# Kernel tuning notes

Hardware: AMD Instinct MI355X
Metric: run time of the kernel (lower is better)

## Reference

```python
import jax, jax.numpy as jnp
import numpy as np

DIM = 128


def setup_inputs() -> dict:
    key = jax.random.key(0)
    k1, k2, k3, k4 = jax.random.split(key, 4)
    x = jax.random.normal(k1, (8, 32768, DIM), dtype=jnp.float32)
    # nn.Linear(dim, dim*3, bias=False): weight applied as x @ W.T; store as [dim, 3*dim]
    W_qkv = jax.random.normal(k2, (DIM, 3 * DIM), dtype=jnp.float32) * (DIM ** -0.5)
    W_out = jax.random.normal(k3, (DIM, DIM), dtype=jnp.float32) * (DIM ** -0.5)
    b_out = jax.random.normal(k4, (DIM,), dtype=jnp.float32) * 0.01
    return {"x": x, "W_qkv": W_qkv, "W_out": W_out, "b_out": b_out}


def reference(x, W_qkv, W_out, b_out):
    dim = x.shape[-1]
    scale = dim ** -0.5
    qkv = x @ W_qkv  # [b, n, 3d]
    q, k, v = jnp.split(qkv, 3, axis=-1)
    q = jax.nn.softmax(q, axis=-1) * scale
    k = jax.nn.softmax(k, axis=-1)
    v = jax.nn.softmax(v, axis=-1)
    context = jnp.einsum('bnd,bne->bde', q, k)  # [b, d, d]
    out = jnp.einsum('bde,bne->bnd', context, v)  # [b, n, d]
    return out @ W_out + b_out
```

## Files before the change

### kernel.cpp

```cpp
#include <hip/hip_runtime.h>

#define SEQ 32768
#define QSCALE 0.08838834764831845f

typedef __attribute__((ext_vector_type(8))) short short8;
typedef __attribute__((ext_vector_type(8))) __bf16 bf16x8;
typedef __attribute__((ext_vector_type(16))) float f32x16;
typedef __attribute__((ext_vector_type(4))) float f32x4;
typedef __attribute__((ext_vector_type(4))) int int4v;
typedef __attribute__((ext_vector_type(2))) int int2v;

#define SWZ(r, c) ((((r) << 7) + (c)) ^ (((r) & 7) << 3))

__device__ __forceinline__ int cvtpk(float lo, float hi) {
  int r;
  asm("v_cvt_pk_bf16_f32 %0, %1, %2" : "=v"(r) : "v"(lo), "v"(hi));
  return r;
}

__device__ __forceinline__ f32x16 mfma_ii(int4v a, int4v b, f32x16 c) {
  return __builtin_amdgcn_mfma_f32_32x32x16_bf16(
      __builtin_bit_cast(bf16x8, a), __builtin_bit_cast(bf16x8, b), c, 0, 0, 0);
}

__device__ __forceinline__ int4v build_frag(float e0, float e1, float e2, float e3,
                                            float e4, float e5, float e6, float e7,
                                            int hi) {
  int t0 = cvtpk(e0, e1), t1 = cvtpk(e2, e3);
  int t2 = cvtpk(e4, e5), t3 = cvtpk(e6, e7);
  const int u0 = __shfl_xor(t2, 32), u1 = __shfl_xor(t3, 32);
  const int u2 = __shfl_xor(t0, 32), u3 = __shfl_xor(t1, 32);
  int4v f;
  f[0] = hi ? u0 : t0;
  f[1] = hi ? u1 : t1;
  f[2] = hi ? t2 : u2;
  f[3] = hi ? t3 : u3;
  return f;
}

__global__ void la_prep(const float* __restrict__ Wqkv, int4v* __restrict__ Wf) {
  const int fid = blockIdx.x * 256 + threadIdx.x;
  if (fid >= 6144) return;
  const int side = fid >> 11;
  const int rem = fid & 2047;
  const int tile = rem >> 9;
  const int ks = (rem >> 6) & 7;
  const int lane = rem & 63;
  const int k0 = ks * 16 + ((lane >> 5) << 3);
  const int col = side * 128 + tile * 32 + (lane & 31);
  int4v f;
  #pragma unroll
  for (int a = 0; a < 4; ++a)
    f[a] = cvtpk(Wqkv[(k0 + 2 * a) * 384 + col], Wqkv[(k0 + 2 * a + 1) * 384 + col]);
  Wf[fid] = f;
}

__global__ __launch_bounds__(1024, 4)
void la_pass1(const float* __restrict__ x, const int4v* __restrict__ Wf,
              float* __restrict__ partials, int strips, int nch) {
  __shared__ __align__(16) short xs[2][64 * 128];
  __shared__ int4v fragbuf[2][2][4][4][64];
  __shared__ __align__(16) float sumbuf[2][2][2][32][4];

  const int tid = threadIdx.x;
  const int lane = tid & 63;
  const int wv = tid >> 6;
  const int l31 = lane & 31;
  const int hi = lane >> 5;
  const int koff = hi << 3;
  const int h = wv >> 3;
  const int c = (wv >> 1) & 3;
  const int rh = wv & 1;
  const int td = wv >> 2;
  const int te = wv & 3;
  const float qs = h ? 1.0f : QSCALE;
  const int b = blockIdx.x / strips;
  const int strip = blockIdx.x - b * strips;
  const long base = (long)b * SEQ + (long)strip * (nch * 64);

  int4v wf[8];
  #pragma unroll
  for (int ks = 0; ks < 8; ++ks)
    wf[ks] = Wf[((((h << 2) + c) << 3) + ks) * 64 + lane];

  const int lr = tid >> 4;
  const int cf = (tid & 15) << 3;
  {
    const float* xp = x + (base + lr) * 128 + cf;
    f32x4 u0 = *(const f32x4*)xp;
    f32x4 u1 = *(const f32x4*)(xp + 4);
    int4v p;
    p[0] = cvtpk(u0[0], u0[1]); p[1] = cvtpk(u0[2], u0[3]);
    p[2] = cvtpk(u1[0], u1[1]); p[3] = cvtpk(u1[2], u1[3]);
    *(int4v*)&xs[0][SWZ(lr, cf)] = p;
  }
  __syncthreads();

  f32x16 ctx = {0.f};
  const int r0 = rh << 5;
  for (int i = 0; i < nch; ++i) {
    const int cur = i & 1;
    const int inx = (i + 1 < nch) ? i + 1 : i;
    const float* xp = x + (base + inx * 64 + lr) * 128 + cf;
    f32x4 u0 = *(const f32x4*)xp;
    f32x4 u1 = *(const f32x4*)(xp + 4);

    f32x16 acc = {0.f};
    #pragma unroll
    for (int ks = 0; ks < 8; ++ks) {
      const int4v xf = *(const int4v*)&xs[cur][SWZ(r0 + l31, (ks << 4) + koff)];
      acc = mfma_ii(wf[ks], xf, acc);
    }
    {
      float sa = 0.f, sb = 0.f;
      #pragma unroll
      for (int r = 0; r < 16; r += 2) { sa += __expf(acc[r]); sb += __expf(acc[r + 1]); }
      float s = sa + sb;
      s += __shfl_xor(s, 32);
      if (!hi) sumbuf[cur][h][rh][l31][c] = s;
    }

    acc = f32x16{0.f};
    #pragma unroll
    for (int ks = 0; ks < 8; ++ks) {
      const int4v xf = *(const int4v*)&xs[cur][SWZ(r0 + l31, (ks << 4) + koff)];
      acc = mfma_ii(xf, wf[ks], acc);
    }
    #pragma unroll
    for (int r = 0; r < 16; ++r) acc[r] = __expf(acc[r]);

    {
      int4v p;
      p[0] = cvtpk(u0[0], u0[1]); p[1] = cvtpk(u0[2], u0[3]);
      p[2] = cvtpk(u1[0], u1[1]); p[3] = cvtpk(u1[2], u1[3]);
      *(int4v*)&xs[cur ^ 1][SWZ(lr, cf)] = p;
    }
    __syncthreads();

    #pragma unroll
    for (int r = 0; r < 16; ++r) {
      const int n = (r & 3) + ((r >> 2) << 3) + (hi << 2);
      const f32x4 sv = *(const f32x4*)&sumbuf[cur][h][rh][n][0];
      acc[r] *= qs * __builtin_amdgcn_rcpf(sv[0] + sv[1] + sv[2] + sv[3]);
    }
    fragbuf[cur][h][c][(rh << 1) + 0][lane] =
        build_frag(acc[0], acc[1], acc[2], acc[3], acc[4], acc[5], acc[6], acc[7], hi);
    fragbuf[cur][h][c][(rh << 1) + 1][lane] =
        build_frag(acc[8], acc[9], acc[10], acc[11], acc[12], acc[13], acc[14], acc[15], hi);

    if (i > 0) {
      const int pb = cur ^ 1;
      #pragma unroll
      for (int ks = 0; ks < 4; ++ks)
        ctx = mfma_ii(fragbuf[pb][0][td][ks][lane], fragbuf[pb][1][te][ks][lane], ctx);
    }
  }
  __syncthreads();
  {
    const int pb = (nch - 1) & 1;
    #pragma unroll
    for (int ks = 0; ks < 4; ++ks)
      ctx = mfma_ii(fragbuf[pb][0][td][ks][lane], fragbuf[pb][1][te][ks][lane], ctx);
  }

  float* pout = partials + (long)blockIdx.x * 16384;
  #pragma unroll
  for (int r = 0; r < 16; ++r) {
    const int drow = (td << 5) + (r & 3) + ((r >> 2) << 3) + (hi << 2);
    pout[(drow << 7) + (te << 5) + l31] = ctx[r];
  }
}

__global__ void la_reduce(const float* __restrict__ partials, float* __restrict__ ctx,
                          int strips) {
  const int b = blockIdx.x >> 4;
  const int sl = blockIdx.x & 15;
  const int idx = (sl << 10) + ((int)threadIdx.x << 2);
  f32x4 acc = {0.f};
  for (int st = 0; st < strips; ++st)
    acc += *(const f32x4*)(partials + ((long)(b * strips + st) << 14) + idx);
  *(f32x4*)(ctx + ((long)b << 14) + idx) = acc;
}

__global__ void la_mkern(const float* __restrict__ ctx, const float* __restrict__ Wout,
                         int4v* __restrict__ Mtf) {
  __shared__ __align__(16) float cl[128 * 132];
  __shared__ float wo[128 * 32];
  const int tid = threadIdx.x;
  const int b = blockIdx.x >> 2;
  const int d0 = (blockIdx.x & 3) << 5;
  const float* cp = ctx + ((long)b << 14);
  for (int i = tid << 2; i < 16384; i += 1024) {
    f32x4 v = *(const f32x4*)(cp + i);
    *(f32x4*)&cl[(i >> 7) * 132 + (i & 127)] = v;
  }
  for (int i = tid; i < 128 * 32; i += 256)
    wo[i] = Wout[((i >> 5) << 7) + d0 + (i & 31)];
  __syncthreads();
  const int dq = tid >> 3;
  const int e0 = (tid & 7) << 4;
  float acc[16];
  #pragma unroll
  for (int i = 0; i < 16; ++i) acc[i] = 0.0f;
  for (int d = 0; d < 128; ++d) {
    const float w = wo[(d << 5) + dq];
    const float* cr = &cl[d * 132 + e0];
    #pragma unroll
    for (int i = 0; i < 16; ++i) acc[i] += cr[i] * w;
  }
  const int dp = d0 + dq;
  const int j = dp & 3, l = dp >> 2, ks = e0 >> 4;
  int4v lo, hi2;
  lo[0] = cvtpk(acc[0], acc[1]);   lo[1] = cvtpk(acc[2], acc[3]);
  lo[2] = cvtpk(acc[4], acc[5]);   lo[3] = cvtpk(acc[6], acc[7]);
  hi2[0] = cvtpk(acc[8], acc[9]);  hi2[1] = cvtpk(acc[10], acc[11]);
  hi2[2] = cvtpk(acc[12], acc[13]); hi2[3] = cvtpk(acc[14], acc[15]);
  int4v* dst = Mtf + ((((long)b << 2) + j) * 8 + ks) * 64;
  dst[l] = lo;
  dst[32 + l] = hi2;
}

__global__ __launch_bounds__(256, 3)
void la_pass2(const float* __restrict__ x, const int4v* __restrict__ Wf,
              const int4v* __restrict__ Mtf, const float* __restrict__ bout,
              float* __restrict__ out) {
  __shared__ __align__(16) short xs[4][32 * 128];

  const int tid = threadIdx.x;
  const int lane = tid & 63;
  const int wv = tid >> 6;
  const int l31 = lane & 31;
  const int hi = lane >> 5;
  const int koff = hi << 3;
  const int b = blockIdx.x >> 8;
  const int chunk = blockIdx.x & 255;
  const long row0 = (long)b * SEQ + (long)chunk * 128 + (wv << 5);

  {
    const float* xb = x + row0 * 128;
    f32x4 u[16];
    #pragma unroll
    for (int t = 0; t < 16; ++t)
      u[t] = *(const f32x4*)(xb + t * 256 + lane * 4);
    #pragma unroll
    for (int t = 0; t < 16; ++t) {
      const int flat = t * 256 + lane * 4;
      int2v w;
      w[0] = cvtpk(u[t][0], u[t][1]);
      w[1] = cvtpk(u[t][2], u[t][3]);
      *(int2v*)&xs[wv][SWZ(flat >> 7, flat & 127)] = w;
    }
  }
  const f32x4 bias = *(const f32x4*)(bout + (l31 << 2));
  asm volatile("s_waitcnt lgkmcnt(0)" ::: "memory");
  __builtin_amdgcn_sched_barrier(0);

  int4v xfr[8];
  #pragma unroll
  for (int ks = 0; ks < 8; ++ks)
    xfr[ks] = *(const int4v*)&xs[wv][SWZ(l31, (ks << 4) + koff)];

  const int4v* WvT = Wf + 2 * 2048;
  f32x16 a0 = {0.f}, a1 = {0.f}, a2 = {0.f}, a3 = {0.f};
  #pragma unroll
  for (int ks = 0; ks < 8; ++ks) {
    a0 = mfma_ii(WvT[(0 * 8 + ks) * 64 + lane], xfr[ks], a0);
    a1 = mfma_ii(WvT[(1 * 8 + ks) * 64 + lane], xfr[ks], a1);
    a2 = mfma_ii(WvT[(2 * 8 + ks) * 64 + lane], xfr[ks], a2);
    a3 = mfma_ii(WvT[(3 * 8 + ks) * 64 + lane], xfr[ks], a3);
  }

  float s = 0.f;
  #pragma unroll
  for (int r = 0; r < 16; ++r) {
    a0[r] = __expf(a0[r]); s += a0[r];
    a1[r] = __expf(a1[r]); s += a1[r];
    a2[r] = __expf(a2[r]); s += a2[r];
    a3[r] = __expf(a3[r]); s += a3[r];
  }
  s += __shfl_xor(s, 32);
  const float inv = __builtin_amdgcn_rcpf(s);
  #pragma unroll
  for (int r = 0; r < 16; ++r) {
    a0[r] *= inv; a1[r] *= inv; a2[r] *= inv; a3[r] *= inv;
  }

  int4v vf[8];
  vf[0] = build_frag(a0[0], a0[1], a0[2], a0[3], a0[4], a0[5], a0[6], a0[7], hi);
  vf[1] = build_frag(a0[8], a0[9], a0[10], a0[11], a0[12], a0[13], a0[14], a0[15], hi);
  vf[2] = build_frag(a1[0], a1[1], a1[2], a1[3], a1[4], a1[5], a1[6], a1[7], hi);
  vf[3] = build_frag(a1[8], a1[9], a1[10], a1[11], a1[12], a1[13], a1[14], a1[15], hi);
  vf[4] = build_frag(a2[0], a2[1], a2[2], a2[3], a2[4], a2[5], a2[6], a2[7], hi);
  vf[5] = build_frag(a2[8], a2[9], a2[10], a2[11], a2[12], a2[13], a2[14], a2[15], hi);
  vf[6] = build_frag(a3[0], a3[1], a3[2], a3[3], a3[4], a3[5], a3[6], a3[7], hi);
  vf[7] = build_frag(a3[8], a3[9], a3[10], a3[11], a3[12], a3[13], a3[14], a3[15], hi);

  const int4v* MtB = Mtf + ((long)b << 11);
  f32x16 o0 = {0.f}, o1 = {0.f}, o2 = {0.f}, o3 = {0.f};
  #pragma unroll
  for (int ks = 0; ks < 8; ++ks) {
    o0 = mfma_ii(vf[ks], MtB[(0 * 8 + ks) * 64 + lane], o0);
    o1 = mfma_ii(vf[ks], MtB[(1 * 8 + ks) * 64 + lane], o1);
    o2 = mfma_ii(vf[ks], MtB[(2 * 8 + ks) * 64 + lane], o2);
    o3 = mfma_ii(vf[ks], MtB[(3 * 8 + ks) * 64 + lane], o3);
  }

  float* obase = out + row0 * 128 + (l31 << 2);
  #pragma unroll
  for (int r = 0; r < 16; ++r) {
    const int n = (r & 3) + ((r >> 2) << 3) + (hi << 2);
    f32x4 v;
    v[0] = o0[r] + bias[0];
    v[1] = o1[r] + bias[1];
    v[2] = o2[r] + bias[2];
    v[3] = o3[r] + bias[3];
    *(f32x4*)(obase + (long)n * 128) = v;
  }
}

extern "C" void kernel_launch(void* const* d_in, const int* in_sizes, int n_in,
                              void* d_out, int out_size, void* d_ws, size_t ws_size,
                              hipStream_t stream) {
  const float* x = (const float*)d_in[0];
  const float* Wqkv = (const float*)d_in[1];
  const float* Wout = (const float*)d_in[2];
  const float* bout = (const float*)d_in[3];
  float* out = (float*)d_out;

  const int strips = 32;
  const int nch = SEQ / (strips * 64);

  float* partials = (float*)d_ws;
  float* ctx = partials + (size_t)8 * strips * 16384;
  int4v* Mtf = (int4v*)(ctx + 8 * 16384);
  int4v* Wf = Mtf + 16384;

  la_prep<<<dim3(24), dim3(256), 0, stream>>>(Wqkv, Wf);
  la_pass1<<<dim3(8 * strips), dim3(1024), 0, stream>>>(x, Wf, partials, strips, nch);
  la_reduce<<<dim3(128), dim3(256), 0, stream>>>(partials, ctx, strips);
  la_mkern<<<dim3(32), dim3(256), 0, stream>>>(ctx, Wout, Mtf);
  la_pass2<<<dim3(2048), dim3(256), 0, stream>>>(x, Wf, Mtf, bout, out);
}
```

Measured before the change: 158.6 us.

## Reuse one QK projection MFMA pass and transpose probabilities through swizzled LDS

```diff
diff --git a/kernel.cpp b/kernel.cpp
--- a/kernel.cpp
+++ b/kernel.cpp
@@ -2,6 +2,7 @@
 
 #define SEQ 32768
 #define QSCALE 0.08838834764831845f
+#define NCH 16
 
 typedef __attribute__((ext_vector_type(8))) short short8;
 typedef __attribute__((ext_vector_type(8))) __bf16 bf16x8;
@@ -11,11 +12,18 @@
 typedef __attribute__((ext_vector_type(2))) int int2v;
 
 #define SWZ(r, c) ((((r) << 7) + (c)) ^ (((r) & 7) << 3))
+#define PSWZ(ch, n) ((((ch) << 6) + (n)) ^ (((ch) & 7) << 3))
 
 __device__ __forceinline__ int cvtpk(float lo, float hi) {
   int r;
   asm("v_cvt_pk_bf16_f32 %0, %1, %2" : "=v"(r) : "v"(lo), "v"(hi));
   return r;
+}
+
+__device__ __forceinline__ short bf16b(float f) {
+  unsigned u = __builtin_bit_cast(unsigned, f);
+  u += 0x7fffu + ((u >> 16) & 1u);
+  return (short)(u >> 16);
 }
 
 __device__ __forceinline__ f32x16 mfma_ii(int4v a, int4v b, f32x16 c) {
@@ -57,9 +65,9 @@
 
 __global__ __launch_bounds__(1024, 4)
 void la_pass1(const float* __restrict__ x, const int4v* __restrict__ Wf,
-              float* __restrict__ partials, int strips, int nch) {
+              float* __restrict__ partials) {
   __shared__ __align__(16) short xs[2][64 * 128];
-  __shared__ int4v fragbuf[2][2][4][4][64];
+  __shared__ __align__(16) short ptile[2][2][128 * 64];
   __shared__ __align__(16) float sumbuf[2][2][2][32][4];
 
   const int tid = threadIdx.x;
@@ -74,9 +82,9 @@
   const int td = wv >> 2;
   const int te = wv & 3;
   const float qs = h ? 1.0f : QSCALE;
-  const int b = blockIdx.x / strips;
-  const int strip = blockIdx.x - b * strips;
-  const long base = (long)b * SEQ + (long)strip * (nch * 64);
+  const int b = blockIdx.x >> 5;
+  const int strip = blockIdx.x & 31;
+  const long base = (long)b * SEQ + (long)strip * (NCH * 64);
 
   int4v wf[8];
   #pragma unroll
@@ -98,9 +106,9 @@
 
   f32x16 ctx = {0.f};
   const int r0 = rh << 5;
-  for (int i = 0; i < nch; ++i) {
+  for (int i = 0; i < NCH; ++i) {
     const int cur = i & 1;
-    const int inx = (i + 1 < nch) ? i + 1 : i;
+    const int inx = (i + 1 < NCH) ? i + 1 : i;
     const float* xp = x + (base + inx * 64 + lr) * 128 + cf;
     f32x4 u0 = *(const f32x4*)xp;
     f32x4 u1 = *(const f32x4*)(xp + 4);
@@ -114,20 +122,14 @@
     {
       float sa = 0.f, sb = 0.f;
       #pragma unroll
-      for (int r = 0; r < 16; r += 2) { sa += __expf(acc[r]); sb += __expf(acc[r + 1]); }
+      for (int r = 0; r < 16; r += 2) {
+        acc[r] = __expf(acc[r]);     sa += acc[r];
+        acc[r + 1] = __expf(acc[r + 1]); sb += acc[r + 1];
+      }
       float s = sa + sb;
       s += __shfl_xor(s, 32);
       if (!hi) sumbuf[cur][h][rh][l31][c] = s;
     }
-
-    acc = f32x16{0.f};
-    #pragma unroll
-    for (int ks = 0; ks < 8; ++ks) {
-      const int4v xf = *(const int4v*)&xs[cur][SWZ(r0 + l31, (ks << 4) + koff)];
-      acc = mfma_ii(xf, wf[ks], acc);
-    }
-    #pragma unroll
-    for (int r = 0; r < 16; ++r) acc[r] = __expf(acc[r]);
 
     {
       int4v p;
@@ -137,30 +139,37 @@
     }
     __syncthreads();
 
-    #pragma unroll
-    for (int r = 0; r < 16; ++r) {
-      const int n = (r & 3) + ((r >> 2) << 3) + (hi << 2);
-      const f32x4 sv = *(const f32x4*)&sumbuf[cur][h][rh][n][0];
-      acc[r] *= qs * __builtin_amdgcn_rcpf(sv[0] + sv[1] + sv[2] + sv[3]);
-    }
-    fragbuf[cur][h][c][(rh << 1) + 0][lane] =
-        build_frag(acc[0], acc[1], acc[2], acc[3], acc[4], acc[5], acc[6], acc[7], hi);
-    fragbuf[cur][h][c][(rh << 1) + 1][lane] =
-        build_frag(acc[8], acc[9], acc[10], acc[11], acc[12], acc[13], acc[14], acc[15], hi);
+    {
+      const f32x4 sv = *(const f32x4*)&sumbuf[cur][h][rh][l31][0];
+      const float invn = qs * __builtin_amdgcn_rcpf(sv[0] + sv[1] + sv[2] + sv[3]);
+      short* pt = &ptile[cur][h][0];
+      const int n = (rh << 5) + l31;
+      #pragma unroll
+      for (int r = 0; r < 16; ++r) {
+        const int ch = (c << 5) + (r & 3) + ((r >> 2) << 3) + (hi << 2);
+        pt[PSWZ(ch, n)] = bf16b(acc[r] * invn);
+      }
+    }
 
     if (i > 0) {
       const int pb = cur ^ 1;
       #pragma unroll
-      for (int ks = 0; ks < 4; ++ks)
-        ctx = mfma_ii(fragbuf[pb][0][td][ks][lane], fragbuf[pb][1][te][ks][lane], ctx);
+      for (int ks = 0; ks < 4; ++ks) {
+        const int4v aq = *(const int4v*)&ptile[pb][0][PSWZ((td << 5) + l31, (ks << 4) + koff)];
+        const int4v bk = *(const int4v*)&ptile[pb][1][PSWZ((te << 5) + l31, (ks << 4) + koff)];
+        ctx = mfma_ii(aq, bk, ctx);
+      }
     }
   }
   __syncthreads();
   {
-    const int pb = (nch - 1) & 1;
-    #pragma unroll
-    for (int ks = 0; ks < 4; ++ks)
-      ctx = mfma_ii(fragbuf[pb][0][td][ks][lane], fragbuf[pb][1][te][ks][lane], ctx);
+    const int pb = (NCH - 1) & 1;
+    #pragma unroll
+    for (int ks = 0; ks < 4; ++ks) {
+      const int4v aq = *(const int4v*)&ptile[pb][0][PSWZ((td << 5) + l31, (ks << 4) + koff)];
+      const int4v bk = *(const int4v*)&ptile[pb][1][PSWZ((te << 5) + l31, (ks << 4) + koff)];
+      ctx = mfma_ii(aq, bk, ctx);
+    }
   }
 
   float* pout = partials + (long)blockIdx.x * 16384;
@@ -328,7 +337,6 @@
   float* out = (float*)d_out;
 
   const int strips = 32;
-  const int nch = SEQ / (strips * 64);
 
   float* partials = (float*)d_ws;
   float* ctx = partials + (size_t)8 * strips * 16384;
@@ -336,7 +344,7 @@
   int4v* Wf = Mtf + 16384;
 
   la_prep<<<dim3(24), dim3(256), 0, stream>>>(Wqkv, Wf);
-  la_pass1<<<dim3(8 * strips), dim3(1024), 0, stream>>>(x, Wf, partials, strips, nch);
+  la_pass1<<<dim3(8 * strips), dim3(1024), 0, stream>>>(x, Wf, partials);
   la_reduce<<<dim3(128), dim3(256), 0, stream>>>(partials, ctx, strips);
   la_mkern<<<dim3(32), dim3(256), 0, stream>>>(ctx, Wout, Mtf);
   la_pass2<<<dim3(2048), dim3(256), 0, stream>>>(x, Wf, Mtf, bout, out);
```

Result: faster. 152.8 us (-3.7%).
